# Optimization experiments

Measured on AMD Instinct MI355X. Metric: run time of the kernel, lower is better.

The kernel has to match this reference:

```python
import jax, jax.numpy as jnp
import numpy as np

IN_F = 2048
OUT_F = 2048
GRID = 5
BATCH = 16384

def setup_inputs() -> dict:
    key = jax.random.key(0)
    kx, kb, ks = jax.random.split(key, 3)
    x = jax.random.normal(kx, (BATCH, IN_F), dtype=jnp.float32)
    # kaiming_uniform_(a=sqrt(5)) on [out, in]: bound = sqrt(6/((1+5)*in)) = 1/sqrt(in)
    bound = 1.0 / np.sqrt(IN_F)
    base_weight = jax.random.uniform(kb, (OUT_F, IN_F), minval=-bound, maxval=bound, dtype=jnp.float32)
    spline_weights = jax.random.uniform(ks, (OUT_F, IN_F, GRID), minval=-0.1, maxval=0.1, dtype=jnp.float32)
    return {"x": x, "base_weight": base_weight, "spline_weights": spline_weights}

def reference(x, base_weight, spline_weights):
    # base path: SiLU then linear (no bias)
    base_out = jnp.einsum('bi,oi->bo', jax.nn.silu(x), base_weight)
    # RBF spline basis over fixed grid in [-1, 1]
    grid = jnp.linspace(-1.0, 1.0, GRID, dtype=x.dtype)  # [g]
    basis = jnp.exp(-((x[..., None] - grid) ** 2) * 5.0)  # [b, i, g]
    spline_out = jnp.einsum('big,oig->bo', basis, spline_weights)
    return base_out + spline_out
```

## Files before the change

kernel.cpp:

```cpp
#include <hip/hip_runtime.h>
#include <hip/hip_bf16.h>
#include <cstdint>
#include <cstddef>


#define KIN 2048
#define NOUT 2048
#define BATCH 16384
#define KEXP 12288
#define NKT 192

typedef __bf16 bf16x8 __attribute__((ext_vector_type(8)));
typedef float f32x4 __attribute__((ext_vector_type(4)));
typedef unsigned short u16x4 __attribute__((ext_vector_type(4)));

__device__ __forceinline__ unsigned short f2bf(float f) {
    union { float f; uint32_t u; } v; v.f = f;
    return (unsigned short)((v.u + 0x7FFFu + ((v.u >> 16) & 1u)) >> 16);
}

__device__ __forceinline__ void load_lds16(const void* gptr, void* lptr) {
    __builtin_amdgcn_global_load_lds(
        (const __attribute__((address_space(1))) unsigned int*)gptr,
        (__attribute__((address_space(3))) unsigned int*)lptr,
        16, 0, 0);
}

__global__ __launch_bounds__(256)
void expand_ab(const float* __restrict__ X, const float* __restrict__ BW,
               const float* __restrict__ SW, __bf16* __restrict__ Aexp,
               __bf16* __restrict__ Wexp)
{
    __shared__ __align__(16) __bf16 rowbuf[KEXP];
    const int bid = blockIdx.x;
    const int tid = threadIdx.x;

    if (bid >= NOUT) {
        const int row = bid - NOUT;
        const float* xrow = X + (size_t)row * KIN;
        const float K0 = 42.521082000062783f;
        const float K1 = 3.4903429574597902f;
        const float K2 = 0.2865047968601901f;
        const float K3 = 0.023517745856009107f;
        #pragma unroll
        for (int s = 0; s < 2; ++s) {
            const f32x4 xv = *(const f32x4*)(xrow + (s * 256 + tid) * 4);
            float o[24];
            #pragma unroll
            for (int e = 0; e < 4; ++e) {
                const float xf = xv[e];
                const float d0 = xf + 1.0f;
                float b = __expf(-5.0f * d0 * d0);
                const float s5 = __expf(5.0f * xf);
                o[e * 6 + 0] = b;
                b *= s5 * K0; o[e * 6 + 1] = b;
                b *= s5 * K1; o[e * 6 + 2] = b;
                b *= s5 * K2; o[e * 6 + 3] = b;
                b *= s5 * K3; o[e * 6 + 4] = b;
                o[e * 6 + 5] = xf / (1.0f + __expf(-xf));
            }
            __bf16* dst = rowbuf + (s * 1024 + tid * 4) * 6;
            #pragma unroll
            for (int q = 0; q < 3; ++q) {
                bf16x8 v;
                #pragma unroll
                for (int t = 0; t < 8; ++t) v[t] = (__bf16)o[q * 8 + t];
                *(bf16x8*)(dst + q * 8) = v;
            }
        }
        __syncthreads();
        bf16x8* out = (bf16x8*)(Aexp + (size_t)row * KEXP);
        const bf16x8* lsrc = (const bf16x8*)rowbuf;
        #pragma unroll
        for (int t = 0; t < 6; ++t)
            out[tid + t * 256] = lsrc[tid + t * 256];
    } else {
        const int orow = bid;
        #pragma unroll
        for (int s = 0; s < 2; ++s) {
            const int i0 = s * 1024 + tid * 4;
            const float* sb = SW + ((size_t)orow * KIN + i0) * 5;
            const f32x4 bw = *(const f32x4*)(BW + (size_t)orow * KIN + i0);
            float sw[20];
            #pragma unroll
            for (int q = 0; q < 5; ++q) {
                const f32x4 v = *(const f32x4*)(sb + q * 4);
                sw[q * 4 + 0] = v.x; sw[q * 4 + 1] = v.y;
                sw[q * 4 + 2] = v.z; sw[q * 4 + 3] = v.w;
            }
            __bf16* dst = rowbuf + (size_t)i0 * 6;
            #pragma unroll
            for (int q = 0; q < 3; ++q) {
                bf16x8 v;
                #pragma unroll
                for (int t = 0; t < 8; ++t) {
                    const int e = (q * 8 + t) / 6;
                    const int c = (q * 8 + t) % 6;
                    v[t] = (c < 5) ? (__bf16)sw[e * 5 + c] : (__bf16)bw[e];
                }
                *(bf16x8*)(dst + q * 8) = v;
            }
        }
        __syncthreads();
        bf16x8* out = (bf16x8*)(Wexp + (size_t)orow * KEXP);
        const bf16x8* lsrc = (const bf16x8*)rowbuf;
        #pragma unroll
        for (int t = 0; t < 6; ++t)
            out[tid + t * 256] = lsrc[tid + t * 256];
    }
}

__global__ __launch_bounds__(512, 2)
void gemm8(const __bf16* __restrict__ A, const __bf16* __restrict__ W,
           float* __restrict__ OUT)
{
    __shared__ __align__(16) __bf16 LDS[65536];
    __bf16* LA = LDS;
    __bf16* LB = LDS + 32768;

    const int tid  = threadIdx.x;
    const int lane = tid & 63;
    const int wave = tid >> 6;
    const int r    = lane & 15;
    const int quad = lane >> 4;
    const int wm   = wave >> 2;
    const int wn   = wave & 3;

    const int bid0 = blockIdx.x;
    const int bid  = (bid0 & 7) * 64 + (bid0 >> 3);
    const int mt  = bid >> 3;
    const int nt  = bid & 7;
    const int m0  = mt * 256;
    const int n0  = nt * 256;

    const int c0   = tid;
    const int c1   = tid + 512;
    const int row0 = c0 >> 2, row1 = c1 >> 2;
    const int j0   = (c0 & 3) ^ ((c0 >> 3) & 3);
    const int j1   = (c1 & 3) ^ ((c1 >> 3) & 3);
    const __bf16* srcA0 = A + (size_t)(m0 + row0) * KEXP + j0 * 8;
    const __bf16* srcA1 = A + (size_t)(m0 + row1) * KEXP + j1 * 8;
    const __bf16* srcB0 = W + (size_t)(n0 + row0) * KEXP + j0 * 8;
    const __bf16* srcB1 = W + (size_t)(n0 + row1) * KEXP + j1 * 8;

    const int dst0 = wave * 512;
    const int dst1 = 4096 + wave * 512;

    const int swz = (quad ^ ((r >> 1) & 3)) * 8;
    const __bf16* a_rd = LA + (wm * 128 + r) * 32 + swz;
    const __bf16* b_rd = LB + (wn * 64 + r) * 32 + swz;

    f32x4 acc[8][4];
    #pragma unroll
    for (int i = 0; i < 8; ++i)
        #pragma unroll
        for (int j = 0; j < 4; ++j)
            acc[i][j] = (f32x4){0.0f, 0.0f, 0.0f, 0.0f};

    bf16x8 afX[4], afY[4], bfA[4], bfB[4];

#define BARX() asm volatile("s_barrier" ::: "memory")
#define VM6()  asm volatile("s_waitcnt vmcnt(6)" ::: "memory")

#define STAGE_A(buf, kh, kt) do { \
    const size_t ko = (size_t)(kt) * 64 + (kh) * 32; \
    load_lds16(srcA0 + ko, LA + ((buf) * 2 + (kh)) * 8192 + dst0); \
    load_lds16(srcA1 + ko, LA + ((buf) * 2 + (kh)) * 8192 + dst1); } while (0)

#define STAGE_B(buf, kh, kt) do { \
    const size_t ko = (size_t)(kt) * 64 + (kh) * 32; \
    load_lds16(srcB0 + ko, LB + ((buf) * 2 + (kh)) * 8192 + dst0); \
    load_lds16(srcB1 + ko, LB + ((buf) * 2 + (kh)) * 8192 + dst1); } while (0)

#define READ_A(arr, buf, ks, a) do { \
    const __bf16* p_ = a_rd + ((buf) * 2 + (ks)) * 8192 + (a) * 2048; \
    arr[0] = *(const bf16x8*)(p_); \
    arr[1] = *(const bf16x8*)(p_ + 512); \
    arr[2] = *(const bf16x8*)(p_ + 1024); \
    arr[3] = *(const bf16x8*)(p_ + 1536); } while (0)

#define READ_BF(arr, buf, ks) do { \
    const __bf16* p_ = b_rd + ((buf) * 2 + (ks)) * 8192; \
    arr[0] = *(const bf16x8*)(p_); \
    arr[1] = *(const bf16x8*)(p_ + 512); \
    arr[2] = *(const bf16x8*)(p_ + 1024); \
    arr[3] = *(const bf16x8*)(p_ + 1536); } while (0)

#define MFMA16(frag, bfr, a) do { \
    __builtin_amdgcn_s_setprio(1); \
    _Pragma("unroll") \
    for (int mi_ = 0; mi_ < 4; ++mi_) { \
        _Pragma("unroll") \
        for (int nj_ = 0; nj_ < 4; ++nj_) \
            acc[(a) * 4 + mi_][nj_] = __builtin_amdgcn_mfma_f32_16x16x32_bf16( \
                frag[mi_], bfr[nj_], acc[(a) * 4 + mi_][nj_], 0, 0, 0); \
    } \
    __builtin_amdgcn_s_setprio(0); } while (0)

    STAGE_B(0, 0, 0); STAGE_A(0, 0, 0); STAGE_B(0, 1, 0); STAGE_A(0, 1, 0);
    STAGE_B(1, 0, 1); STAGE_A(1, 0, 1); STAGE_B(1, 1, 1);
    VM6();
    BARX();
    READ_A(afX, 0, 0, 0);
    READ_BF(bfA, 0, 0);

    for (int t = 0; t < 96; ++t) {
        const int kt1 = 2 * t + 1;
        const int sA  = (2 * t + 2 < NKT) ? 2 * t + 2 : NKT - 1;
        const int sB  = (2 * t + 3 < NKT) ? 2 * t + 3 : NKT - 1;

        STAGE_A(1, 1, kt1);
        BARX();
        READ_A(afY, 0, 0, 1);
        MFMA16(afX, bfA, 0);
        STAGE_B(0, 0, sA);
        READ_A(afX, 0, 1, 0);
        READ_BF(bfB, 0, 1);
        MFMA16(afY, bfA, 1);
        BARX();

        STAGE_A(0, 0, sA);
        BARX();
        READ_A(afY, 0, 1, 1);
        MFMA16(afX, bfB, 0);
        STAGE_B(0, 1, sA);
        VM6();
        MFMA16(afY, bfB, 1);
        BARX();

        STAGE_A(0, 1, sA);
        READ_A(afX, 1, 0, 0);
        READ_BF(bfA, 1, 0);
        BARX();
        READ_A(afY, 1, 0, 1);
        MFMA16(afX, bfA, 0);
        STAGE_B(1, 0, sB);
        READ_A(afX, 1, 1, 0);
        READ_BF(bfB, 1, 1);
        MFMA16(afY, bfA, 1);
        BARX();

        STAGE_A(1, 0, sB);
        BARX();
        READ_A(afY, 1, 1, 1);
        MFMA16(afX, bfB, 0);
        STAGE_B(1, 1, sB);
        VM6();
        MFMA16(afY, bfB, 1);
        BARX();

        READ_A(afX, 0, 0, 0);
        READ_BF(bfA, 0, 0);
    }

    #pragma unroll
    for (int fi = 0; fi < 8; ++fi) {
        #pragma unroll
        for (int nj = 0; nj < 4; ++nj) {
            const int col  = n0 + wn * 64 + nj * 16 + r;
            const int rowb = m0 + wm * 128 + fi * 16 + quad * 4;
            #pragma unroll
            for (int reg = 0; reg < 4; ++reg)
                OUT[(size_t)(rowb + reg) * NOUT + col] = acc[fi][nj][reg];
        }
    }
#undef BARX
#undef VM6
#undef STAGE_A
#undef STAGE_B
#undef READ_A
#undef READ_BF
#undef MFMA16
}

#define BM 128
#define BN 128
#define NF 16
#define BK 96
#define LDK 104

__global__ __launch_bounds__(256)
void kan_fused(const float* __restrict__ X, const float* __restrict__ BW,
               const float* __restrict__ SW, float* __restrict__ OUT)
{
    __shared__ __align__(16) unsigned short As[BM * LDK];
    __shared__ __align__(16) unsigned short Bs[BN * LDK];

    const int tid  = threadIdx.x;
    const int lane = tid & 63;
    const int wave = tid >> 6;
    const int mt = blockIdx.x >> 4;
    const int nt = blockIdx.x & 15;
    const int m0 = mt * BM;
    const int n0 = nt * BN;
    const int r    = lane & 15;
    const int quad = lane >> 4;
    const int wm = (wave & 1) * 64;
    const int wn = (wave >> 1) * 64;

    f32x4 acc[4][4];
    #pragma unroll
    for (int i = 0; i < 4; ++i)
        #pragma unroll
        for (int j = 0; j < 4; ++j)
            acc[i][j] = (f32x4){0.0f, 0.0f, 0.0f, 0.0f};

    for (int it = 0; it < KIN / NF; ++it) {
        const int i0 = it * NF;
        __syncthreads();
        #pragma unroll
        for (int s = 0; s < 2; ++s) {
            const int slot = tid + s * 256;
            const int row  = slot >> 2;
            const int fq   = slot & 3;
            const f32x4 xv = *(const f32x4*)(X + (size_t)(m0 + row) * KIN + i0 + fq * 4);
            unsigned short basv[20];
            unsigned short silv[4];
            #pragma unroll
            for (int e = 0; e < 4; ++e) {
                const float xf = xv[e];
                silv[e] = f2bf(xf / (1.0f + __expf(-xf)));
                #pragma unroll
                for (int c = 0; c < 5; ++c) {
                    const float d = xf - (-1.0f + 0.5f * (float)c);
                    basv[e * 5 + c] = f2bf(__expf(-5.0f * d * d));
                }
            }
            unsigned short* dst = As + row * LDK + fq * 20;
            #pragma unroll
            for (int q = 0; q < 5; ++q) {
                u16x4 v;
                v.x = basv[q * 4 + 0]; v.y = basv[q * 4 + 1];
                v.z = basv[q * 4 + 2]; v.w = basv[q * 4 + 3];
                *(u16x4*)(dst + q * 4) = v;
            }
            u16x4 sv;
            sv.x = silv[0]; sv.y = silv[1]; sv.z = silv[2]; sv.w = silv[3];
            *(u16x4*)(As + row * LDK + 80 + fq * 4) = sv;
        }
        {
            const int orow = tid >> 1;
            const int half = tid & 1;
            const float* sbase = SW + (size_t)(n0 + orow) * (KIN * 5) + i0 * 5 + half * 40;
            unsigned short* brow = Bs + orow * LDK + half * 40;
            #pragma unroll
            for (int p = 0; p < 10; ++p) {
                const f32x4 wv = *(const f32x4*)(sbase + p * 4);
                u16x4 v;
                v.x = f2bf(wv.x); v.y = f2bf(wv.y);
                v.z = f2bf(wv.z); v.w = f2bf(wv.w);
                *(u16x4*)(brow + p * 4) = v;
            }
        }
        #pragma unroll
        for (int s = 0; s < 2; ++s) {
            const int slot = tid + s * 256;
            const int row  = slot >> 2;
            const int fq   = slot & 3;
            const f32x4 wv = *(const f32x4*)(BW + (size_t)(n0 + row) * KIN + i0 + fq * 4);
            u16x4 v;
            v.x = f2bf(wv.x); v.y = f2bf(wv.y);
            v.z = f2bf(wv.z); v.w = f2bf(wv.w);
            *(u16x4*)(Bs + row * LDK + 80 + fq * 4) = v;
        }
        __syncthreads();
        #pragma unroll
        for (int ks = 0; ks < 3; ++ks) {
            bf16x8 af[4], bfr[4];
            #pragma unroll
            for (int mi = 0; mi < 4; ++mi)
                af[mi] = *(const bf16x8*)(As + (wm + mi * 16 + r) * LDK + ks * 32 + quad * 8);
            #pragma unroll
            for (int ni = 0; ni < 4; ++ni)
                bfr[ni] = *(const bf16x8*)(Bs + (wn + ni * 16 + r) * LDK + ks * 32 + quad * 8);
            #pragma unroll
            for (int mi = 0; mi < 4; ++mi)
                #pragma unroll
                for (int ni = 0; ni < 4; ++ni)
                    acc[mi][ni] = __builtin_amdgcn_mfma_f32_16x16x32_bf16(
                        af[mi], bfr[ni], acc[mi][ni], 0, 0, 0);
        }
    }
    #pragma unroll
    for (int mi = 0; mi < 4; ++mi) {
        #pragma unroll
        for (int ni = 0; ni < 4; ++ni) {
            const int col  = n0 + wn + ni * 16 + r;
            const int rowb = m0 + wm + mi * 16 + quad * 4;
            #pragma unroll
            for (int reg = 0; reg < 4; ++reg)
                OUT[(size_t)(rowb + reg) * NOUT + col] = acc[mi][ni][reg];
        }
    }
}

extern "C" void kernel_launch(void* const* d_in, const int* in_sizes, int n_in,
                              void* d_out, int out_size, void* d_ws, size_t ws_size,
                              hipStream_t stream) {
    const float* X  = (const float*)d_in[0];
    const float* BW = (const float*)d_in[1];
    const float* SW = (const float*)d_in[2];
    float* OUT = (float*)d_out;

    const size_t nA = (size_t)BATCH * KEXP;
    const size_t nW = (size_t)NOUT * KEXP;
    const size_t ws_need = (nA + nW) * sizeof(__bf16);

    if (ws_size >= ws_need) {
        __bf16* Aexp = (__bf16*)d_ws;
        __bf16* Wexp = Aexp + nA;
        expand_ab<<<dim3(NOUT + BATCH), dim3(256), 0, stream>>>(X, BW, SW, Aexp, Wexp);
        gemm8<<<dim3(512), dim3(512), 0, stream>>>(Aexp, Wexp, OUT);
    } else {
        kan_fused<<<dim3(128 * 16), dim3(256), 0, stream>>>(X, BW, SW, OUT);
    }
}
```

Measured before the change: 963.6 us.

## Load B fragments directly from global into registers, bypassing LDS

The weight operand B is no longer staged through LDS. Each wave reads its bf16x8 B fragments straight from global memory into registers, which halves LDS usage and removes several barriers per iteration. The cost is that each wave (the two wm waves sharing a column slab) issues its own uncoalesced global loads for B, with no reuse through LDS. It also relies on the waitcnt ordering to cover global load latency.

```diff
diff --git a/kernel.cpp b/kernel.cpp
--- a/kernel.cpp
+++ b/kernel.cpp
@@ -114,9 +114,7 @@
 void gemm8(const __bf16* __restrict__ A, const __bf16* __restrict__ W,
            float* __restrict__ OUT)
 {
-    __shared__ __align__(16) __bf16 LDS[65536];
-    __bf16* LA = LDS;
-    __bf16* LB = LDS + 32768;
+    __shared__ __align__(16) __bf16 LA[32768];
 
     const int tid  = threadIdx.x;
     const int lane = tid & 63;
@@ -140,15 +138,17 @@
     const int j1   = (c1 & 3) ^ ((c1 >> 3) & 3);
     const __bf16* srcA0 = A + (size_t)(m0 + row0) * KEXP + j0 * 8;
     const __bf16* srcA1 = A + (size_t)(m0 + row1) * KEXP + j1 * 8;
-    const __bf16* srcB0 = W + (size_t)(n0 + row0) * KEXP + j0 * 8;
-    const __bf16* srcB1 = W + (size_t)(n0 + row1) * KEXP + j1 * 8;
 
     const int dst0 = wave * 512;
     const int dst1 = 4096 + wave * 512;
 
     const int swz = (quad ^ ((r >> 1) & 3)) * 8;
     const __bf16* a_rd = LA + (wm * 128 + r) * 32 + swz;
-    const __bf16* b_rd = LB + (wn * 64 + r) * 32 + swz;
+
+    const __bf16* bB0 = W + (size_t)(n0 + wn * 64 +  0 + r) * KEXP + quad * 8;
+    const __bf16* bB1 = W + (size_t)(n0 + wn * 64 + 16 + r) * KEXP + quad * 8;
+    const __bf16* bB2 = W + (size_t)(n0 + wn * 64 + 32 + r) * KEXP + quad * 8;
+    const __bf16* bB3 = W + (size_t)(n0 + wn * 64 + 48 + r) * KEXP + quad * 8;
 
     f32x4 acc[8][4];
     #pragma unroll
@@ -167,20 +167,14 @@
     load_lds16(srcA0 + ko, LA + ((buf) * 2 + (kh)) * 8192 + dst0); \
     load_lds16(srcA1 + ko, LA + ((buf) * 2 + (kh)) * 8192 + dst1); } while (0)
 
-#define STAGE_B(buf, kh, kt) do { \
-    const size_t ko = (size_t)(kt) * 64 + (kh) * 32; \
-    load_lds16(srcB0 + ko, LB + ((buf) * 2 + (kh)) * 8192 + dst0); \
-    load_lds16(srcB1 + ko, LB + ((buf) * 2 + (kh)) * 8192 + dst1); } while (0)
+#define LOADB(arr, ko) do { \
+    arr[0] = *(const bf16x8*)(bB0 + (ko)); \
+    arr[1] = *(const bf16x8*)(bB1 + (ko)); \
+    arr[2] = *(const bf16x8*)(bB2 + (ko)); \
+    arr[3] = *(const bf16x8*)(bB3 + (ko)); } while (0)
 
 #define READ_A(arr, buf, ks, a) do { \
     const __bf16* p_ = a_rd + ((buf) * 2 + (ks)) * 8192 + (a) * 2048; \
-    arr[0] = *(const bf16x8*)(p_); \
-    arr[1] = *(const bf16x8*)(p_ + 512); \
-    arr[2] = *(const bf16x8*)(p_ + 1024); \
-    arr[3] = *(const bf16x8*)(p_ + 1536); } while (0)
-
-#define READ_BF(arr, buf, ks) do { \
-    const __bf16* p_ = b_rd + ((buf) * 2 + (ks)) * 8192; \
     arr[0] = *(const bf16x8*)(p_); \
     arr[1] = *(const bf16x8*)(p_ + 512); \
     arr[2] = *(const bf16x8*)(p_ + 1024); \
@@ -197,60 +191,55 @@
     } \
     __builtin_amdgcn_s_setprio(0); } while (0)
 
-    STAGE_B(0, 0, 0); STAGE_A(0, 0, 0); STAGE_B(0, 1, 0); STAGE_A(0, 1, 0);
-    STAGE_B(1, 0, 1); STAGE_A(1, 0, 1); STAGE_B(1, 1, 1);
-    VM6();
+    STAGE_A(0, 0, 0); STAGE_A(0, 1, 0); STAGE_A(1, 0, 1);
+    LOADB(bfA, 0);
+    asm volatile("s_waitcnt vmcnt(4)" ::: "memory");
     BARX();
     READ_A(afX, 0, 0, 0);
-    READ_BF(bfA, 0, 0);
 
     for (int t = 0; t < 96; ++t) {
         const int kt1 = 2 * t + 1;
         const int sA  = (2 * t + 2 < NKT) ? 2 * t + 2 : NKT - 1;
         const int sB  = (2 * t + 3 < NKT) ? 2 * t + 3 : NKT - 1;
+        const size_t kb  = (size_t)t * 128;
+        const size_t kb5 = (kb + 128 <= (size_t)(NKT - 1) * 64)
+                               ? kb + 128 : (size_t)(NKT - 1) * 64;
 
         STAGE_A(1, 1, kt1);
-        BARX();
+        LOADB(bfB, kb + 32);
         READ_A(afY, 0, 0, 1);
+        VM6();
         MFMA16(afX, bfA, 0);
-        STAGE_B(0, 0, sA);
         READ_A(afX, 0, 1, 0);
-        READ_BF(bfB, 0, 1);
         MFMA16(afY, bfA, 1);
         BARX();
 
         STAGE_A(0, 0, sA);
-        BARX();
+        LOADB(bfA, kb + 64);
         READ_A(afY, 0, 1, 1);
+        VM6();
         MFMA16(afX, bfB, 0);
-        STAGE_B(0, 1, sA);
-        VM6();
+        READ_A(afX, 1, 0, 0);
         MFMA16(afY, bfB, 1);
         BARX();
 
         STAGE_A(0, 1, sA);
-        READ_A(afX, 1, 0, 0);
-        READ_BF(bfA, 1, 0);
-        BARX();
+        LOADB(bfB, kb + 96);
         READ_A(afY, 1, 0, 1);
+        VM6();
         MFMA16(afX, bfA, 0);
-        STAGE_B(1, 0, sB);
         READ_A(afX, 1, 1, 0);
-        READ_BF(bfB, 1, 1);
         MFMA16(afY, bfA, 1);
         BARX();
 
         STAGE_A(1, 0, sB);
-        BARX();
+        LOADB(bfA, kb5);
         READ_A(afY, 1, 1, 1);
+        VM6();
         MFMA16(afX, bfB, 0);
-        STAGE_B(1, 1, sB);
-        VM6();
+        READ_A(afX, 0, 0, 0);
         MFMA16(afY, bfB, 1);
         BARX();
-
-        READ_A(afX, 0, 0, 0);
-        READ_BF(bfA, 0, 0);
     }
 
     #pragma unroll
@@ -267,9 +256,8 @@
 #undef BARX
 #undef VM6
 #undef STAGE_A
-#undef STAGE_B
+#undef LOADB
 #undef READ_A
-#undef READ_BF
 #undef MFMA16
 }
 
```

Result: slower. 1.503 ms (+56.0%).
